# Kernel tuning notes

Measured on AMD Instinct MI355X. Metric: run time of the kernel, lower is better.

The kernel has to match this reference:

```python
import jax, jax.numpy as jnp
import numpy as np

D_MODEL = 1024
NUM_HEADS = 16
D_K = D_MODEL // NUM_HEADS


def setup_inputs() -> dict:
    key = jax.random.key(0)
    ks = jax.random.split(key, 8)
    s = 1.0 / np.sqrt(D_MODEL)
    inp = {
        'q': jax.random.normal(ks[0], (2, 2048, D_MODEL), jnp.float32),
        'k': jax.random.normal(ks[1], (2, 2048, D_MODEL), jnp.float32),
        'v': jax.random.normal(ks[2], (2, 2048, D_MODEL), jnp.float32),
        'Wq': jax.random.normal(ks[3], (D_MODEL, D_MODEL), jnp.float32) * s,
        'bq': jnp.zeros((D_MODEL,), jnp.float32),
        'Wk': jax.random.normal(ks[4], (D_MODEL, D_MODEL), jnp.float32) * s,
        'bk': jnp.zeros((D_MODEL,), jnp.float32),
        'Wv': jax.random.normal(ks[5], (D_MODEL, D_MODEL), jnp.float32) * s,
        'bv': jnp.zeros((D_MODEL,), jnp.float32),
        'Wo': jax.random.normal(ks[6], (D_MODEL, D_MODEL), jnp.float32) * s,
        'bo': jnp.zeros((D_MODEL,), jnp.float32),
    }
    return inp


def _split_heads(x):
    # [B, S, D] -> [B, H, S, d_k]
    b, s, _ = x.shape
    return x.reshape(b, s, NUM_HEADS, D_K).transpose(0, 2, 1, 3)


def reference(q, k, v, Wq, bq, Wk, bk, Wv, bv, Wo, bo):
    qh = _split_heads(q @ Wq + bq)
    kh = _split_heads(k @ Wk + bk)
    vh = _split_heads(v @ Wv + bv)
    scale = 1.0 / jnp.sqrt(jnp.asarray(D_K, qh.dtype))
    scores = jnp.einsum('bhqd,bhkd->bhqk', qh, kh) * scale  # [B,H,S,S]
    probs = jax.nn.softmax(scores, axis=-1)
    ctx = jnp.einsum('bhqk,bhkd->bhqd', probs, vh)
    b, h, s, d = ctx.shape
    ctx = ctx.transpose(0, 2, 1, 3).reshape(b, s, h * d)
    return ctx @ Wo + bo
```

## Files before the change

kernel.cpp:

```cpp
#include <hip/hip_runtime.h>

#define D_MODEL 1024
#define SEQ     2048
#define BATCH   2
#define NH      16
#define DK      64
#define MROWS   (BATCH*SEQ)

typedef __attribute__((ext_vector_type(8))) short short8;
typedef __attribute__((ext_vector_type(4))) float f32x4;

#define QSCALE 0.18033688011112042f

#if __has_builtin(__builtin_amdgcn_exp2f)
#define EXP2(x) __builtin_amdgcn_exp2f(x)
#else
#define EXP2(x) exp2f(x)
#endif

static __device__ __forceinline__ unsigned short f2bf(float f) {
  unsigned u = __float_as_uint(f);
  u += 0x7fff + ((u >> 16) & 1);
  return (unsigned short)(u >> 16);
}

static __device__ __forceinline__ unsigned pack_bf2(float a, float b) {
  unsigned ua = __float_as_uint(a) + 0x8000u;
  unsigned ub = __float_as_uint(b) + 0x8000u;
#if __has_builtin(__builtin_amdgcn_perm)
  return __builtin_amdgcn_perm(ub, ua, 0x07060302u);
#else
  return (ua >> 16) | (ub & 0xffff0000u);
#endif
}

static __device__ __forceinline__ void load16_lds(const void* g, void* l) {
  __builtin_amdgcn_global_load_lds(
      (const __attribute__((address_space(1))) void*)g,
      (__attribute__((address_space(3))) void*)l, 16, 0, 0);
}

__global__ void cvt_all(const float* __restrict__ q, const float* __restrict__ k,
                        const float* __restrict__ v, unsigned short* __restrict__ out, int n4) {
  int i = blockIdx.x * blockDim.x + threadIdx.x;
  if (i >= n4) return;
  const float* src = (blockIdx.y == 0) ? q : (blockIdx.y == 1) ? k : v;
  float4 val = ((const float4*)src)[i];
  unsigned r0 = (unsigned)f2bf(val.x) | ((unsigned)f2bf(val.y) << 16);
  unsigned r1 = (unsigned)f2bf(val.z) | ((unsigned)f2bf(val.w) << 16);
  uint2 u; u.x = r0; u.y = r1;
  ((uint2*)(out + (size_t)blockIdx.y * MROWS * D_MODEL))[i] = u;
}

__global__ void wtrans_all(const float* __restrict__ Wq, const float* __restrict__ Wk,
                           const float* __restrict__ Wv, const float* __restrict__ Wo,
                           unsigned short* __restrict__ Wt) {
  __shared__ float t[32][33];
  const float* W = (blockIdx.z == 0) ? Wq : (blockIdx.z == 1) ? Wk
                 : (blockIdx.z == 2) ? Wv : Wo;
  unsigned short* dst = Wt + (size_t)blockIdx.z * D_MODEL * D_MODEL;
  int n0 = blockIdx.x * 32, k0 = blockIdx.y * 32;
  int tx = threadIdx.x & 31, ty = threadIdx.x >> 5;
#pragma unroll
  for (int i = 0; i < 32; i += 8)
    t[ty + i][tx] = W[(size_t)(k0 + ty + i) * D_MODEL + n0 + tx];
  __syncthreads();
#pragma unroll
  for (int i = 0; i < 32; i += 8)
    dst[(size_t)(n0 + ty + i) * D_MODEL + k0 + tx] = f2bf(t[tx][ty + i]);
}

__global__ __launch_bounds__(256, 2) void gemm_qkv(
    const unsigned short* __restrict__ Abig,
    const unsigned short* __restrict__ Wt,
    const float* __restrict__ bq, const float* __restrict__ bk, const float* __restrict__ bv,
    unsigned short* __restrict__ Qh, unsigned short* __restrict__ Kh,
    unsigned short* __restrict__ Vt)
{
  constexpr int K = D_MODEL;
  __shared__ unsigned short As[128 * 32];
  __shared__ unsigned short Bs[128 * 32];
  const int g = blockIdx.y >> 5;
  const unsigned short* A  = Abig + (size_t)g * MROWS * K;
  const unsigned short* Bt = Wt + (size_t)g * K * K;
  const float* bias = (g == 0) ? bq : (g == 1) ? bk : bv;
  unsigned short* out = (g == 0) ? Qh : (g == 1) ? Kh : Vt;

  const int tid  = threadIdx.x;
  const int wave = tid >> 6, lane = tid & 63;
  const int quad = lane >> 4, l16 = lane & 15;
  const int bm = (blockIdx.y & 31) * 128, bn = blockIdx.x * 128;
  const int wm = (wave >> 1) * 64, wn = (wave & 1) * 64;
  const int srow = tid >> 2, scol = (tid & 3) * 8;

  f32x4 acc[4][4] = {};
  for (int k0 = 0; k0 < K; k0 += 32) {
    load16_lds(&A [(size_t)(bm      + srow) * K + k0 + scol], &As[tid * 8]);
    load16_lds(&A [(size_t)(bm + 64 + srow) * K + k0 + scol], &As[2048 + tid * 8]);
    load16_lds(&Bt[(size_t)(bn      + srow) * K + k0 + scol], &Bs[tid * 8]);
    load16_lds(&Bt[(size_t)(bn + 64 + srow) * K + k0 + scol], &Bs[2048 + tid * 8]);
    __syncthreads();
    short8 af[4], bfr[4];
#pragma unroll
    for (int i = 0; i < 4; ++i) {
      af[i]  = *(const short8*)&As[(wm + i * 16 + l16) * 32 + quad * 8];
      bfr[i] = *(const short8*)&Bs[(wn + i * 16 + l16) * 32 + quad * 8];
    }
#pragma unroll
    for (int mt = 0; mt < 4; ++mt)
#pragma unroll
      for (int nt = 0; nt < 4; ++nt)
        acc[mt][nt] = __builtin_amdgcn_mfma_f32_16x16x32_bf16(af[mt], bfr[nt], acc[mt][nt], 0, 0, 0);
    __syncthreads();
  }

  if (g == 2) {
    float* tb = (float*)As + wave * 272;
#pragma unroll
    for (int mt = 0; mt < 4; ++mt)
#pragma unroll
      for (int nt = 0; nt < 4; ++nt) {
        int nbase = bn + wn + nt * 16;
        float bvv = bias[nbase + l16];
#pragma unroll
        for (int r = 0; r < 4; ++r)
          tb[(quad * 4 + r) * 17 + l16] = acc[mt][nt][r] + bvv;
        float v2[4];
#pragma unroll
        for (int r2 = 0; r2 < 4; ++r2)
          v2[r2] = tb[l16 * 17 + quad * 4 + r2];
        int m = bm + wm + mt * 16 + l16;
        int bb = m >> 11, s = m & 2047;
#pragma unroll
        for (int r2 = 0; r2 < 4; ++r2) {
          int n = nbase + quad * 4 + r2;
          int h = n >> 6, d = n & 63;
          out[((size_t)(bb * NH + h) * DK + d) * SEQ + s] = f2bf(v2[r2]);
        }
      }
    return;
  }

  const float scl = (g == 0) ? QSCALE : 1.0f;
#pragma unroll
  for (int mt = 0; mt < 4; ++mt)
#pragma unroll
    for (int nt = 0; nt < 4; ++nt) {
      int n = bn + wn + nt * 16 + l16;
      float bvv = bias[n];
#pragma unroll
      for (int r = 0; r < 4; ++r) {
        int m = bm + wm + mt * 16 + quad * 4 + r;
        float v = (acc[mt][nt][r] + bvv) * scl;
        int b = m >> 11, s = m & 2047;
        int h = n >> 6,  d = n & 63;
        out[((size_t)(b * NH + h) * SEQ + s) * DK + d] = f2bf(v);
      }
    }
}

__global__ __launch_bounds__(256, 2) void gemm_out(
    const unsigned short* __restrict__ A,
    const unsigned short* __restrict__ Bt,
    const float* __restrict__ bias,
    float* __restrict__ out)
{
  constexpr int K = D_MODEL;
  __shared__ unsigned short As[128 * 32];
  __shared__ unsigned short Bs[64 * 32];
  const int tid  = threadIdx.x;
  const int wave = tid >> 6, lane = tid & 63;
  const int quad = lane >> 4, l16 = lane & 15;
  const int bm = blockIdx.y * 128, bn = blockIdx.x * 64;
  const int wm = (wave >> 1) * 64, wn = (wave & 1) * 32;
  const int srow = tid >> 2, scol = (tid & 3) * 8;

  f32x4 acc[4][2] = {};
  for (int k0 = 0; k0 < K; k0 += 32) {
    load16_lds(&A [(size_t)(bm      + srow) * K + k0 + scol], &As[tid * 8]);
    load16_lds(&A [(size_t)(bm + 64 + srow) * K + k0 + scol], &As[2048 + tid * 8]);
    load16_lds(&Bt[(size_t)(bn      + srow) * K + k0 + scol], &Bs[tid * 8]);
    __syncthreads();
    short8 af[4], bfr[2];
#pragma unroll
    for (int i = 0; i < 4; ++i)
      af[i]  = *(const short8*)&As[(wm + i * 16 + l16) * 32 + quad * 8];
#pragma unroll
    for (int i = 0; i < 2; ++i)
      bfr[i] = *(const short8*)&Bs[(wn + i * 16 + l16) * 32 + quad * 8];
#pragma unroll
    for (int mt = 0; mt < 4; ++mt)
#pragma unroll
      for (int nt = 0; nt < 2; ++nt)
        acc[mt][nt] = __builtin_amdgcn_mfma_f32_16x16x32_bf16(af[mt], bfr[nt], acc[mt][nt], 0, 0, 0);
    __syncthreads();
  }
#pragma unroll
  for (int mt = 0; mt < 4; ++mt)
#pragma unroll
    for (int nt = 0; nt < 2; ++nt) {
      int n = bn + wn + nt * 16 + l16;
      float bvv = bias[n];
#pragma unroll
      for (int r = 0; r < 4; ++r) {
        int m = bm + wm + mt * 16 + quad * 4 + r;
        out[(size_t)m * D_MODEL + n] = acc[mt][nt][r] + bvv;
      }
    }
}

__global__ __launch_bounds__(256) void attn(
    const unsigned short* __restrict__ Qh,
    const unsigned short* __restrict__ Kh,
    const unsigned short* __restrict__ Vt,
    unsigned short* __restrict__ ctx)
{
  const int blk = blockIdx.x;
  const int bh = blk >> 4, qt = blk & 15;
  const int tid = threadIdx.x, wave = tid >> 6, lane = tid & 63;
  const int quad = lane >> 4, l16 = lane & 15;
  const int r0 = tid >> 3, u = tid & 7;

  __shared__ unsigned short Ks[2][64 * 64];
  __shared__ unsigned short Vs[2][64 * 64];
  __shared__ unsigned short Ps[4][32 * 64];
  __shared__ float Al[4][32];

  const unsigned short* Kbase = Kh + (size_t)bh * SEQ * DK;
  const unsigned short* Vbase = Vt + (size_t)bh * DK * SEQ;
  const unsigned short* Qp = Qh + ((size_t)bh * SEQ + qt * 128 + wave * 32) * DK;

  short8 aq[2][2];
#pragma unroll
  for (int mt = 0; mt < 2; ++mt)
#pragma unroll
    for (int ks = 0; ks < 2; ++ks)
      aq[mt][ks] = *(const short8*)&Qp[(mt * 16 + l16) * DK + ks * 32 + quad * 8];

  f32x4 cacc[2][4] = {};
  float lacc[2] = {0.f, 0.f};

  const int koff0 = ((quad + l16) & 7) * 8;
  const int koff1 = ((4 + quad + l16) & 7) * 8;

  short8 sk0, sk1, sv0, sv1;
  auto stage_load = [&](int c) {
    const unsigned short* kg = Kbase + ((size_t)(c * 64 + r0)) * DK + u * 8;
    sk0 = *(const short8*)kg;
    sk1 = *(const short8*)(kg + (size_t)32 * DK);
    const unsigned short* vg = Vbase + (size_t)r0 * SEQ + c * 64 + u * 8;
    sv0 = *(const short8*)vg;
    sv1 = *(const short8*)(vg + (size_t)32 * SEQ);
  };
  auto stage_write = [&](int b) {
    int p = ((u + r0) & 7) * 8;
    *(short8*)&Ks[b][r0 * 64 + p]        = sk0;
    *(short8*)&Ks[b][(r0 + 32) * 64 + p] = sk1;
    *(short8*)&Vs[b][r0 * 64 + p]        = sv0;
    *(short8*)&Vs[b][(r0 + 32) * 64 + p] = sv1;
  };

  stage_load(0); stage_write(0);
  __syncthreads();

  for (int c = 0; c < SEQ / 64; ++c) {
    const int buf = c & 1;
    const bool pre = (c + 1 < SEQ / 64);
    if (pre) stage_load(c + 1);

    f32x4 s_[2][4] = {};
#pragma unroll
    for (int kt = 0; kt < 4; ++kt) {
      short8 kb0 = *(const short8*)&Ks[buf][(kt * 16 + l16) * 64 + koff0];
      short8 kb1 = *(const short8*)&Ks[buf][(kt * 16 + l16) * 64 + koff1];
      s_[0][kt] = __builtin_amdgcn_mfma_f32_16x16x32_bf16(kb0, aq[0][0], s_[0][kt], 0, 0, 0);
      s_[0][kt] = __builtin_amdgcn_mfma_f32_16x16x32_bf16(kb1, aq[0][1], s_[0][kt], 0, 0, 0);
      s_[1][kt] = __builtin_amdgcn_mfma_f32_16x16x32_bf16(kb0, aq[1][0], s_[1][kt], 0, 0, 0);
      s_[1][kt] = __builtin_amdgcn_mfma_f32_16x16x32_bf16(kb1, aq[1][1], s_[1][kt], 0, 0, 0);
    }

#pragma unroll
    for (int mt = 0; mt < 2; ++mt) {
      float p[4][4];
#pragma unroll
      for (int kt = 0; kt < 4; ++kt)
#pragma unroll
        for (int r = 0; r < 4; ++r)
          p[kt][r] = EXP2(s_[mt][kt][r]);
      float t0 = (p[0][0] + p[0][1]) + (p[0][2] + p[0][3]);
      float t1 = (p[1][0] + p[1][1]) + (p[1][2] + p[1][3]);
      float t2 = (p[2][0] + p[2][1]) + (p[2][2] + p[2][3]);
      float t3 = (p[3][0] + p[3][1]) + (p[3][2] + p[3][3]);
      lacc[mt] += (t0 + t1) + (t2 + t3);
      const int row = mt * 16 + l16;
#pragma unroll
      for (int kt = 0; kt < 4; ++kt) {
        uint2 pk;
        pk.x = pack_bf2(p[kt][0], p[kt][1]);
        pk.y = pack_bf2(p[kt][2], p[kt][3]);
        int pos16 = (kt * 2 + (quad >> 1) + l16) & 7;
        *(uint2*)&Ps[wave][row * 64 + pos16 * 8 + (quad & 1) * 4] = pk;
      }
    }

    {
      short8 ap00 = *(const short8*)&Ps[wave][l16 * 64        + koff0];
      short8 ap01 = *(const short8*)&Ps[wave][l16 * 64        + koff1];
      short8 ap10 = *(const short8*)&Ps[wave][(16 + l16) * 64 + koff0];
      short8 ap11 = *(const short8*)&Ps[wave][(16 + l16) * 64 + koff1];
#pragma unroll
      for (int dt = 0; dt < 4; ++dt) {
        short8 vb0 = *(const short8*)&Vs[buf][(dt * 16 + l16) * 64 + koff0];
        short8 vb1 = *(const short8*)&Vs[buf][(dt * 16 + l16) * 64 + koff1];
        cacc[0][dt] = __builtin_amdgcn_mfma_f32_16x16x32_bf16(ap00, vb0, cacc[0][dt], 0, 0, 0);
        cacc[0][dt] = __builtin_amdgcn_mfma_f32_16x16x32_bf16(ap01, vb1, cacc[0][dt], 0, 0, 0);
        cacc[1][dt] = __builtin_amdgcn_mfma_f32_16x16x32_bf16(ap10, vb0, cacc[1][dt], 0, 0, 0);
        cacc[1][dt] = __builtin_amdgcn_mfma_f32_16x16x32_bf16(ap11, vb1, cacc[1][dt], 0, 0, 0);
      }
    }

    if (pre) {
      stage_write(buf ^ 1);
      __syncthreads();
    }
  }

#pragma unroll
  for (int mt = 0; mt < 2; ++mt) {
    lacc[mt] += __shfl_xor(lacc[mt], 16);
    lacc[mt] += __shfl_xor(lacc[mt], 32);
  }
  if (quad == 0) {
    Al[wave][l16]      = lacc[0];
    Al[wave][16 + l16] = lacc[1];
  }
  const int b = bh >> 4, h = bh & 15;
#pragma unroll
  for (int mt = 0; mt < 2; ++mt) {
    f32x4 lv = *(const f32x4*)&Al[wave][mt * 16 + quad * 4];
#pragma unroll
    for (int r = 0; r < 4; ++r) lv[r] = 1.0f / lv[r];
#pragma unroll
    for (int dt = 0; dt < 4; ++dt)
#pragma unroll
      for (int r = 0; r < 4; ++r) {
        int m = qt * 128 + wave * 32 + mt * 16 + quad * 4 + r;
        float v = cacc[mt][dt][r] * lv[r];
        ctx[(size_t)(b * SEQ + m) * D_MODEL + h * DK + dt * 16 + l16] = f2bf(v);
      }
  }
}

extern "C" void kernel_launch(void* const* d_in, const int* in_sizes, int n_in,
                              void* d_out, int out_size, void* d_ws, size_t ws_size,
                              hipStream_t stream) {
  const float* q  = (const float*)d_in[0];
  const float* k  = (const float*)d_in[1];
  const float* v  = (const float*)d_in[2];
  const float* Wq = (const float*)d_in[3];
  const float* bq = (const float*)d_in[4];
  const float* Wk = (const float*)d_in[5];
  const float* bk = (const float*)d_in[6];
  const float* Wv = (const float*)d_in[7];
  const float* bv = (const float*)d_in[8];
  const float* Wo = (const float*)d_in[9];
  const float* bo = (const float*)d_in[10];

  char* ws = (char*)d_ws;
  const size_t SZ_ACT = (size_t)MROWS * D_MODEL * 2;
  const size_t SZ_W   = (size_t)D_MODEL * D_MODEL * 2;
  unsigned short* qkvb = (unsigned short*)(ws);
  unsigned short* Wall = (unsigned short*)(ws + 3 * SZ_ACT);
  unsigned short* Qh   = (unsigned short*)(ws + 3 * SZ_ACT + 4 * SZ_W);
  unsigned short* Kh   = (unsigned short*)(ws + 4 * SZ_ACT + 4 * SZ_W);
  unsigned short* Vt   = (unsigned short*)(ws + 5 * SZ_ACT + 4 * SZ_W);
  unsigned short* Wot  = Wall + 3 * (size_t)D_MODEL * D_MODEL;
  unsigned short* ctx  = qkvb;

  int n4 = MROWS * D_MODEL / 4;
  cvt_all<<<dim3(n4 / 256, 3), 256, 0, stream>>>(q, k, v, qkvb, n4);
  wtrans_all<<<dim3(32, 32, 4), 256, 0, stream>>>(Wq, Wk, Wv, Wo, Wall);

  gemm_qkv<<<dim3(D_MODEL / 128, 96), 256, 0, stream>>>(qkvb, Wall, bq, bk, bv, Qh, Kh, Vt);

  attn<<<dim3(32 * 16), 256, 0, stream>>>(Qh, Kh, Vt, ctx);

  gemm_out<<<dim3(D_MODEL / 64, MROWS / 128), 256, 0, stream>>>(ctx, Wot, bo, (float*)d_out);
}
```

Measured before the change: 229.2 us.

## Halve attention query tile to double grid size; raise qkv GEMM occupancy bound

The attention kernel now gives each block 64 query rows (16 per wave) instead of 128, doubling the grid from 512 to 1024 blocks. The goal is to fill the 256 CUs better and raise occupancy through fewer registers and a smaller P buffer in shared memory. The row-sum normalisation now uses a lane shuffle instead of a shared-memory round trip. The cost is that every K/V tile is loaded and staged twice as often per query row, which lowers MFMA reuse of each K/V fragment. The QKV GEMM launch bound also rises to 3 waves per SIMD, which may force register spills.

After: 234.8 us. 1.02x slower.

```diff
diff --git a/kernel.cpp b/kernel.cpp
--- a/kernel.cpp
+++ b/kernel.cpp
@@ -70,7 +70,7 @@
     dst[(size_t)(n0 + ty + i) * D_MODEL + k0 + tx] = f2bf(t[tx][ty + i]);
 }
 
-__global__ __launch_bounds__(256, 2) void gemm_qkv(
+__global__ __launch_bounds__(256, 3) void gemm_qkv(
     const unsigned short* __restrict__ Abig,
     const unsigned short* __restrict__ Wt,
     const float* __restrict__ bq, const float* __restrict__ bk, const float* __restrict__ bv,
@@ -216,29 +216,24 @@
     unsigned short* __restrict__ ctx)
 {
   const int blk = blockIdx.x;
-  const int bh = blk >> 4, qt = blk & 15;
+  const int bh = blk >> 5, qt = blk & 31;
   const int tid = threadIdx.x, wave = tid >> 6, lane = tid & 63;
   const int quad = lane >> 4, l16 = lane & 15;
   const int r0 = tid >> 3, u = tid & 7;
 
   __shared__ unsigned short Ks[2][64 * 64];
   __shared__ unsigned short Vs[2][64 * 64];
-  __shared__ unsigned short Ps[4][32 * 64];
-  __shared__ float Al[4][32];
+  __shared__ unsigned short Ps[4][16 * 64];
 
   const unsigned short* Kbase = Kh + (size_t)bh * SEQ * DK;
   const unsigned short* Vbase = Vt + (size_t)bh * DK * SEQ;
-  const unsigned short* Qp = Qh + ((size_t)bh * SEQ + qt * 128 + wave * 32) * DK;
-
-  short8 aq[2][2];
-#pragma unroll
-  for (int mt = 0; mt < 2; ++mt)
-#pragma unroll
-    for (int ks = 0; ks < 2; ++ks)
-      aq[mt][ks] = *(const short8*)&Qp[(mt * 16 + l16) * DK + ks * 32 + quad * 8];
-
-  f32x4 cacc[2][4] = {};
-  float lacc[2] = {0.f, 0.f};
+  const unsigned short* Qp = Qh + ((size_t)bh * SEQ + qt * 64 + wave * 16) * DK;
+
+  short8 aq0 = *(const short8*)&Qp[l16 * DK + quad * 8];
+  short8 aq1 = *(const short8*)&Qp[l16 * DK + 32 + quad * 8];
+
+  f32x4 cacc[4] = {};
+  float lacc = 0.f;
 
   const int koff0 = ((quad + l16) & 7) * 8;
   const int koff1 = ((4 + quad + l16) & 7) * 8;
@@ -268,54 +263,46 @@
     const bool pre = (c + 1 < SEQ / 64);
     if (pre) stage_load(c + 1);
 
-    f32x4 s_[2][4] = {};
+    f32x4 s_[4] = {};
 #pragma unroll
     for (int kt = 0; kt < 4; ++kt) {
       short8 kb0 = *(const short8*)&Ks[buf][(kt * 16 + l16) * 64 + koff0];
       short8 kb1 = *(const short8*)&Ks[buf][(kt * 16 + l16) * 64 + koff1];
-      s_[0][kt] = __builtin_amdgcn_mfma_f32_16x16x32_bf16(kb0, aq[0][0], s_[0][kt], 0, 0, 0);
-      s_[0][kt] = __builtin_amdgcn_mfma_f32_16x16x32_bf16(kb1, aq[0][1], s_[0][kt], 0, 0, 0);
-      s_[1][kt] = __builtin_amdgcn_mfma_f32_16x16x32_bf16(kb0, aq[1][0], s_[1][kt], 0, 0, 0);
-      s_[1][kt] = __builtin_amdgcn_mfma_f32_16x16x32_bf16(kb1, aq[1][1], s_[1][kt], 0, 0, 0);
-    }
-
-#pragma unroll
-    for (int mt = 0; mt < 2; ++mt) {
-      float p[4][4];
-#pragma unroll
-      for (int kt = 0; kt < 4; ++kt)
-#pragma unroll
-        for (int r = 0; r < 4; ++r)
-          p[kt][r] = EXP2(s_[mt][kt][r]);
+      s_[kt] = __builtin_amdgcn_mfma_f32_16x16x32_bf16(kb0, aq0, s_[kt], 0, 0, 0);
+      s_[kt] = __builtin_amdgcn_mfma_f32_16x16x32_bf16(kb1, aq1, s_[kt], 0, 0, 0);
+    }
+
+    float p[4][4];
+#pragma unroll
+    for (int kt = 0; kt < 4; ++kt)
+#pragma unroll
+      for (int r = 0; r < 4; ++r)
+        p[kt][r] = EXP2(s_[kt][r]);
+    {
       float t0 = (p[0][0] + p[0][1]) + (p[0][2] + p[0][3]);
       float t1 = (p[1][0] + p[1][1]) + (p[1][2] + p[1][3]);
       float t2 = (p[2][0] + p[2][1]) + (p[2][2] + p[2][3]);
       float t3 = (p[3][0] + p[3][1]) + (p[3][2] + p[3][3]);
-      lacc[mt] += (t0 + t1) + (t2 + t3);
-      const int row = mt * 16 + l16;
-#pragma unroll
-      for (int kt = 0; kt < 4; ++kt) {
-        uint2 pk;
-        pk.x = pack_bf2(p[kt][0], p[kt][1]);
-        pk.y = pack_bf2(p[kt][2], p[kt][3]);
-        int pos16 = (kt * 2 + (quad >> 1) + l16) & 7;
-        *(uint2*)&Ps[wave][row * 64 + pos16 * 8 + (quad & 1) * 4] = pk;
-      }
+      lacc += (t0 + t1) + (t2 + t3);
+    }
+#pragma unroll
+    for (int kt = 0; kt < 4; ++kt) {
+      uint2 pk;
+      pk.x = pack_bf2(p[kt][0], p[kt][1]);
+      pk.y = pack_bf2(p[kt][2], p[kt][3]);
+      int pos16 = (kt * 2 + (quad >> 1) + l16) & 7;
+      *(uint2*)&Ps[wave][l16 * 64 + pos16 * 8 + (quad & 1) * 4] = pk;
     }
 
     {
-      short8 ap00 = *(const short8*)&Ps[wave][l16 * 64        + koff0];
-      short8 ap01 = *(const short8*)&Ps[wave][l16 * 64        + koff1];
-      short8 ap10 = *(const short8*)&Ps[wave][(16 + l16) * 64 + koff0];
-      short8 ap11 = *(const short8*)&Ps[wave][(16 + l16) * 64 + koff1];
+      short8 ap0 = *(const short8*)&Ps[wave][l16 * 64 + koff0];
+      short8 ap1 = *(const short8*)&Ps[wave][l16 * 64 + koff1];
 #pragma unroll
       for (int dt = 0; dt < 4; ++dt) {
         short8 vb0 = *(const short8*)&Vs[buf][(dt * 16 + l16) * 64 + koff0];
         short8 vb1 = *(const short8*)&Vs[buf][(dt * 16 + l16) * 64 + koff1];
-        cacc[0][dt] = __builtin_amdgcn_mfma_f32_16x16x32_bf16(ap00, vb0, cacc[0][dt], 0, 0, 0);
-        cacc[0][dt] = __builtin_amdgcn_mfma_f32_16x16x32_bf16(ap01, vb1, cacc[0][dt], 0, 0, 0);
-        cacc[1][dt] = __builtin_amdgcn_mfma_f32_16x16x32_bf16(ap10, vb0, cacc[1][dt], 0, 0, 0);
-        cacc[1][dt] = __builtin_amdgcn_mfma_f32_16x16x32_bf16(ap11, vb1, cacc[1][dt], 0, 0, 0);
+        cacc[dt] = __builtin_amdgcn_mfma_f32_16x16x32_bf16(ap0, vb0, cacc[dt], 0, 0, 0);
+        cacc[dt] = __builtin_amdgcn_mfma_f32_16x16x32_bf16(ap1, vb1, cacc[dt], 0, 0, 0);
       }
     }
 
@@ -325,30 +312,21 @@
     }
   }
 
-#pragma unroll
-  for (int mt = 0; mt < 2; ++mt) {
-    lacc[mt] += __shfl_xor(lacc[mt], 16);
-    lacc[mt] += __shfl_xor(lacc[mt], 32);
-  }
-  if (quad == 0) {
-    Al[wave][l16]      = lacc[0];
-    Al[wave][16 + l16] = lacc[1];
-  }
+  lacc += __shfl_xor(lacc, 16);
+  lacc += __shfl_xor(lacc, 32);
   const int b = bh >> 4, h = bh & 15;
-#pragma unroll
-  for (int mt = 0; mt < 2; ++mt) {
-    f32x4 lv = *(const f32x4*)&Al[wave][mt * 16 + quad * 4];
-#pragma unroll
-    for (int r = 0; r < 4; ++r) lv[r] = 1.0f / lv[r];
-#pragma unroll
-    for (int dt = 0; dt < 4; ++dt)
-#pragma unroll
-      for (int r = 0; r < 4; ++r) {
-        int m = qt * 128 + wave * 32 + mt * 16 + quad * 4 + r;
-        float v = cacc[mt][dt][r] * lv[r];
-        ctx[(size_t)(b * SEQ + m) * D_MODEL + h * DK + dt * 16 + l16] = f2bf(v);
-      }
-  }
+  float lv[4];
+#pragma unroll
+  for (int r = 0; r < 4; ++r)
+    lv[r] = 1.0f / __shfl(lacc, quad * 4 + r);
+#pragma unroll
+  for (int dt = 0; dt < 4; ++dt)
+#pragma unroll
+    for (int r = 0; r < 4; ++r) {
+      int m = qt * 64 + wave * 16 + quad * 4 + r;
+      float v = cacc[dt][r] * lv[r];
+      ctx[(size_t)(b * SEQ + m) * D_MODEL + h * DK + dt * 16 + l16] = f2bf(v);
+    }
 }
 
 extern "C" void kernel_launch(void* const* d_in, const int* in_sizes, int n_in,
@@ -383,7 +361,7 @@
 
   gemm_qkv<<<dim3(D_MODEL / 128, 96), 256, 0, stream>>>(qkvb, Wall, bq, bk, bv, Qh, Kh, Vt);
 
-  attn<<<dim3(32 * 16), 256, 0, stream>>>(Qh, Kh, Vt, ctx);
+  attn<<<dim3(32 * 32), 256, 0, stream>>>(Qh, Kh, Vt, ctx);
 
   gemm_out<<<dim3(D_MODEL / 64, MROWS / 128), 256, 0, stream>>>(ctx, Wot, bo, (float*)d_out);
 }
```
